# Kernel tuning notes

Hardware: AMD Instinct MI355X
Metric: run time of the kernel (lower is better)

## Reference

```python
import jax, jax.numpy as jnp
import numpy as np

N = 50000
E = 800000
IN_C = 128
OUT_C = 128
N_TYPES = 3
NEG_SLOPE = 0.2  # PyG GATConv default negative_slope


def setup_inputs() -> dict:
    key = jax.random.key(0)
    ks = jax.random.split(key, 10)
    x = jax.random.normal(ks[0], (N, IN_C), dtype=jnp.float32)
    edge_index = jax.random.randint(ks[1], (2, E), 0, N, dtype=jnp.int32)
    edge_type = jax.random.randint(ks[2], (E,), 0, N_TYPES, dtype=jnp.int32)
    node_type = jax.random.randint(ks[3], (N,), 0, 3, dtype=jnp.int32)
    s = 1.0 / np.sqrt(IN_C)
    emb_table = jax.random.normal(ks[4], (3, IN_C), dtype=jnp.float32)
    W = jax.random.normal(ks[5], (N_TYPES, IN_C, OUT_C), dtype=jnp.float32) * s
    att_src = jax.random.normal(ks[6], (N_TYPES, OUT_C), dtype=jnp.float32) * s
    att_dst = jax.random.normal(ks[7], (N_TYPES, OUT_C), dtype=jnp.float32) * s
    bias = jax.random.normal(ks[8], (N_TYPES, OUT_C), dtype=jnp.float32) * 0.01
    return {"x": x, "edge_index": edge_index, "edge_type": edge_type,
            "node_type": node_type, "emb_table": emb_table, "W": W,
            "att_src": att_src, "att_dst": att_dst, "bias": bias}


def reference(x, edge_index, edge_type, node_type, emb_table, W, att_src, att_dst, bias):
    # Eval mode: dropouts are identity. edge_index is non-empty -> GAT branch.
    n = x.shape[0]
    x = x + emb_table[node_type]  # node-type embedding add
    src, dst = edge_index[0], edge_index[1]
    out_sum = jnp.zeros((n, OUT_C), dtype=x.dtype)
    for t in range(N_TYPES):  # per-edge-type GATConv (heads=1, add_self_loops=True)
        xw = x @ W[t]                       # [N, out]
        a_s = xw @ att_src[t]               # [N] alpha_src per node
        a_d = xw @ att_dst[t]               # [N] alpha_dst per node
        mask = edge_type == t               # [E]
        e_raw = jax.nn.leaky_relu(a_s[src] + a_d[dst], NEG_SLOPE)  # [E]
        e_self = jax.nn.leaky_relu(a_s + a_d, NEG_SLOPE)           # [N] self-loop logit
        e_masked = jnp.where(mask, e_raw, -jnp.inf)
        m = jnp.maximum(jax.ops.segment_max(e_masked, dst, num_segments=n), e_self)
        m = jax.lax.stop_gradient(m)
        w_edge = jnp.where(mask, jnp.exp(e_raw - m[dst]), 0.0)     # [E]
        w_self = jnp.exp(e_self - m)                               # [N]
        denom = jax.ops.segment_sum(w_edge, dst, num_segments=n) + w_self
        num = jax.ops.segment_sum(w_edge[:, None] * xw[src], dst, num_segments=n) \
              + w_self[:, None] * xw
        out_sum = out_sum + num / denom[:, None] + bias[t]
        # (attention weights per type are w_edge/denom[dst]; only node output returned)
    return out_sum
```

## Files before the change

kernel.cpp:

```cpp
#include <hip/hip_runtime.h>
#include <math.h>

#define N_NODES 50000
#define N_EDGES 800000
#define C 128
#define NT 3
#define NEG 0.2f
#define CAP 64

#define GEMM_XB 782

typedef __attribute__((ext_vector_type(8))) short short8;
typedef __attribute__((ext_vector_type(4))) float f32x4;

__device__ __forceinline__ float leaky(float v) { return v > 0.f ? v : NEG * v; }

__device__ __forceinline__ unsigned short f2bf(float f) {
  unsigned int u = __float_as_uint(f);
  u = (u + 0x7FFFu + ((u >> 16) & 1u)) >> 16;
  return (unsigned short)u;
}
__device__ __forceinline__ float bf_lo(unsigned int w) { return __uint_as_float(w << 16); }
__device__ __forceinline__ float bf_hi(unsigned int w) { return __uint_as_float(w & 0xFFFF0000u); }

__global__ void k_wt(const float* __restrict__ W, unsigned short* __restrict__ Wt) {
  int idx = blockIdx.x * 256 + threadIdx.x;
  int t = idx >> 14, rem = idx & 16383;
  int n = rem >> 7, k = rem & 127;
  Wt[((size_t)t * C + n) * C + k] = f2bf(W[((size_t)t * C + k) * C + n]);
}

__global__ void k_main(const float* __restrict__ x, const int* __restrict__ node_type,
                       const float* __restrict__ emb, const unsigned short* __restrict__ Wt,
                       unsigned short* __restrict__ xwb,
                       const float* __restrict__ att_src, const float* __restrict__ att_dst,
                       float* __restrict__ a_s, float2* __restrict__ ad_es,
                       const int* __restrict__ ei, const int* __restrict__ etype,
                       int* __restrict__ cnt, int* __restrict__ buckets) {
  __shared__ unsigned short As[64][136];
  __shared__ unsigned short Bs[128][136];
  const int bid = blockIdx.x;
  const int r = bid & 3;
  const int tid = threadIdx.x;

  if (r == 3) {
    int e0 = ((bid >> 2) * 256 + tid) * 4;
    if (e0 + 4 <= N_EDGES) {
      int4 s4 = *(const int4*)(ei + e0);
      int4 d4 = *(const int4*)(ei + N_EDGES + e0);
      int4 t4 = *(const int4*)(etype + e0);
      int p0 = atomicAdd(&cnt[d4.x], 1);
      int p1 = atomicAdd(&cnt[d4.y], 1);
      int p2 = atomicAdd(&cnt[d4.z], 1);
      int p3 = atomicAdd(&cnt[d4.w], 1);
      if (p0 < CAP) buckets[(size_t)d4.x * CAP + p0] = t4.x * N_NODES + s4.x;
      if (p1 < CAP) buckets[(size_t)d4.y * CAP + p1] = t4.y * N_NODES + s4.y;
      if (p2 < CAP) buckets[(size_t)d4.z * CAP + p2] = t4.z * N_NODES + s4.z;
      if (p3 < CAP) buckets[(size_t)d4.w * CAP + p3] = t4.w * N_NODES + s4.w;
    }
    return;
  }

  const int wid = tid >> 6, lane = tid & 63;
  const int m = lane & 15, quad = lane >> 4;
  const int row0 = (bid >> 2) * 64;
  const int t = r;

#pragma unroll
  for (int it = 0; it < 8; ++it) {
    int c = tid + it * 256;
    int rr = c >> 5, q = c & 31;
    int row = row0 + rr;
    float4 xv = make_float4(0.f, 0.f, 0.f, 0.f);
    int nt = 0;
    if (row < N_NODES) {
      xv = *(const float4*)(x + (size_t)row * C + q * 4);
      nt = node_type[row];
    }
    float4 ev = ((const float4*)emb)[nt * 32 + q];
    ushort4 o;
    o.x = f2bf(xv.x + ev.x); o.y = f2bf(xv.y + ev.y);
    o.z = f2bf(xv.z + ev.z); o.w = f2bf(xv.w + ev.w);
    *(ushort4*)&As[rr][q * 4] = o;
  }
  const unsigned short* Wtt = Wt + (size_t)t * C * C;
#pragma unroll
  for (int it = 0; it < 8; ++it) {
    int c = tid + it * 256;
    int n = c >> 4, kc = c & 15;
    *(uint4*)&Bs[n][kc * 8] = *(const uint4*)(Wtt + (size_t)n * C + kc * 8);
  }
  __syncthreads();

  f32x4 acc[8] = {};
#pragma unroll
  for (int k0 = 0; k0 < 128; k0 += 32) {
    short8 a = *(const short8*)&As[wid * 16 + m][k0 + quad * 8];
#pragma unroll
    for (int j = 0; j < 8; ++j) {
      short8 b = *(const short8*)&Bs[j * 16 + m][k0 + quad * 8];
      acc[j] = __builtin_amdgcn_mfma_f32_16x16x32_bf16(a, b, acc[j], 0, 0, 0);
    }
  }

  float asv[8], adv[8];
#pragma unroll
  for (int j = 0; j < 8; ++j) {
    asv[j] = att_src[t * C + j * 16 + m];
    adv[j] = att_dst[t * C + j * 16 + m];
  }
  float ps[4] = {}, pd[4] = {};
#pragma unroll
  for (int j = 0; j < 8; ++j) {
#pragma unroll
    for (int reg = 0; reg < 4; ++reg) {
      int row = row0 + wid * 16 + quad * 4 + reg;
      float v = acc[j][reg];
      if (row < N_NODES) xwb[((size_t)t * N_NODES + row) * C + j * 16 + m] = f2bf(v);
      ps[reg] += v * asv[j];
      pd[reg] += v * adv[j];
    }
  }
#pragma unroll
  for (int off = 1; off < 16; off <<= 1) {
#pragma unroll
    for (int reg = 0; reg < 4; ++reg) {
      ps[reg] += __shfl_xor(ps[reg], off);
      pd[reg] += __shfl_xor(pd[reg], off);
    }
  }
  if (m == 0) {
#pragma unroll
    for (int reg = 0; reg < 4; ++reg) {
      int row = row0 + wid * 16 + quad * 4 + reg;
      if (row < N_NODES) {
        int idx = t * N_NODES + row;
        a_s[idx] = ps[reg];
        ad_es[idx] = make_float2(pd[reg], leaky(ps[reg] + pd[reg]));
      }
    }
  }
}

__global__ void k_gather(const int* __restrict__ cnt, const int* __restrict__ buckets,
                         const unsigned short* __restrict__ xwb,
                         const float* __restrict__ a_s, const float2* __restrict__ ad_es,
                         const float* __restrict__ bias, float* __restrict__ out) {
  int wid = threadIdx.x >> 6;
  int lane = threadIdx.x & 63;
  int i = blockIdx.x * 4 + wid;
  if (i >= N_NODES) return;
  int n = cnt[i];
  if (n > CAP) n = CAP;

  int idxl = 0;
  if (lane < n) idxl = buckets[(size_t)i * CAP + lane];
  int tl = idxl >= 2 * N_NODES ? 2 : (idxl >= N_NODES ? 1 : 0);
  float as = a_s[idxl];
  float2 am = ad_es[tl * N_NODES + i];
  float wl = (lane < n) ? __expf(leaky(as + am.x) - am.y) : 0.f;

  float s0 = tl == 0 ? wl : 0.f;
  float s1 = tl == 1 ? wl : 0.f;
  float s2 = tl == 2 ? wl : 0.f;
#pragma unroll
  for (int off = 1; off < 64; off <<= 1) {
    s0 += __shfl_xor(s0, off);
    s1 += __shfl_xor(s1, off);
    s2 += __shfl_xor(s2, off);
  }
  float inv3[NT] = {1.f / (s0 + 1.f), 1.f / (s1 + 1.f), 1.f / (s2 + 1.f)};
  float wc = wl * inv3[tl];

  float acc0 = 0.f, acc1 = 0.f;
#pragma unroll
  for (int t = 0; t < NT; ++t) {
    int idx = t * N_NODES + i;
    float coef = inv3[t];
    unsigned int w = ((const unsigned int*)(xwb + (size_t)idx * C))[lane];
    float2 b2 = ((const float2*)(bias + t * C))[lane];
    acc0 += coef * bf_lo(w) + b2.x;
    acc1 += coef * bf_hi(w) + b2.y;
  }

  const unsigned int* xwu = (const unsigned int*)xwb;
  int j = 0;
  for (; j + 16 <= n; j += 16) {
    float ac0 = 0.f, ac1 = 0.f;
#pragma unroll
    for (int k = 0; k < 16; ++k) {
      int idx = __shfl(idxl, j + k);
      float c = __shfl(wc, j + k);
      unsigned int v = xwu[(size_t)idx * (C / 2) + lane];
      ac0 += c * bf_lo(v);
      ac1 += c * bf_hi(v);
    }
    acc0 += ac0; acc1 += ac1;
  }
  for (; j + 8 <= n; j += 8) {
    float ac0 = 0.f, ac1 = 0.f;
#pragma unroll
    for (int k = 0; k < 8; ++k) {
      int idx = __shfl(idxl, j + k);
      float c = __shfl(wc, j + k);
      unsigned int v = xwu[(size_t)idx * (C / 2) + lane];
      ac0 += c * bf_lo(v);
      ac1 += c * bf_hi(v);
    }
    acc0 += ac0; acc1 += ac1;
  }
  for (; j < n; ++j) {
    int idx = __shfl(idxl, j);
    float c = __shfl(wc, j);
    unsigned int v = xwu[(size_t)idx * (C / 2) + lane];
    acc0 += c * bf_lo(v);
    acc1 += c * bf_hi(v);
  }
  ((float2*)(out + (size_t)i * C))[lane] = make_float2(acc0, acc1);
}

extern "C" void kernel_launch(void* const* d_in, const int* in_sizes, int n_in,
                              void* d_out, int out_size, void* d_ws, size_t ws_size,
                              hipStream_t stream) {
  const float* x       = (const float*)d_in[0];
  const int* edge_idx  = (const int*)d_in[1];
  const int* edge_type = (const int*)d_in[2];
  const int* node_type = (const int*)d_in[3];
  const float* emb     = (const float*)d_in[4];
  const float* W       = (const float*)d_in[5];
  const float* att_src = (const float*)d_in[6];
  const float* att_dst = (const float*)d_in[7];
  const float* bias    = (const float*)d_in[8];
  float* out = (float*)d_out;

  unsigned short* xwb = (unsigned short*)d_ws;
  unsigned short* Wt  = xwb + (size_t)NT * N_NODES * C;
  float*  a_s   = (float*)(Wt + (size_t)NT * C * C);
  float2* ad_es = (float2*)(a_s + (size_t)NT * N_NODES);
  int*    cnt   = (int*)(ad_es + (size_t)NT * N_NODES);
  int*    buckets = (int*)(cnt + N_NODES);

  hipMemsetAsync(cnt, 0, N_NODES * sizeof(int), stream);
  k_wt<<<192, 256, 0, stream>>>(W, Wt);

  k_main<<<4 * GEMM_XB, 256, 0, stream>>>(x, node_type, emb, Wt, xwb, att_src, att_dst,
                                          a_s, ad_es, edge_idx, edge_type, cnt, buckets);

  k_gather<<<(N_NODES + 3) / 4, 256, 0, stream>>>(cnt, buckets, xwb, a_s, ad_es, bias, out);
}
```

Before: 195.1 us.

## Reuse input tile across all edge types and fold count reset into prep

The main kernel now loads and converts each 64-row x tile once into shared memory. It then loops over the three edge types, reloading only the per-type weight tile between them. Before, three separate blocks each re-read and re-converted the same x rows. The hipMemsetAsync of the per-node counters is folded into the weight-transpose kernel, removing one launch. The trade-off is fewer, longer GEMM blocks with extra barriers, which may reduce parallelism and latency hiding.

```diff
diff --git a/kernel.cpp b/kernel.cpp
--- a/kernel.cpp
+++ b/kernel.cpp
@@ -23,11 +23,18 @@
 __device__ __forceinline__ float bf_lo(unsigned int w) { return __uint_as_float(w << 16); }
 __device__ __forceinline__ float bf_hi(unsigned int w) { return __uint_as_float(w & 0xFFFF0000u); }
 
-__global__ void k_wt(const float* __restrict__ W, unsigned short* __restrict__ Wt) {
-  int idx = blockIdx.x * 256 + threadIdx.x;
-  int t = idx >> 14, rem = idx & 16383;
-  int n = rem >> 7, k = rem & 127;
-  Wt[((size_t)t * C + n) * C + k] = f2bf(W[((size_t)t * C + k) * C + n]);
+__global__ void k_prep(const float* __restrict__ W, unsigned short* __restrict__ Wt,
+                       int* __restrict__ cnt) {
+  int bid = blockIdx.x;
+  if (bid < 192) {
+    int idx = bid * 256 + threadIdx.x;
+    int t = idx >> 14, rem = idx & 16383;
+    int n = rem >> 7, k = rem & 127;
+    Wt[((size_t)t * C + n) * C + k] = f2bf(W[((size_t)t * C + k) * C + n]);
+  } else {
+    int i4 = (bid - 192) * 256 + threadIdx.x;
+    if (i4 < N_NODES / 4) ((int4*)cnt)[i4] = make_int4(0, 0, 0, 0);
+  }
 }
 
 __global__ void k_main(const float* __restrict__ x, const int* __restrict__ node_type,
@@ -40,11 +47,10 @@
   __shared__ unsigned short As[64][136];
   __shared__ unsigned short Bs[128][136];
   const int bid = blockIdx.x;
-  const int r = bid & 3;
   const int tid = threadIdx.x;
 
-  if (r == 3) {
-    int e0 = ((bid >> 2) * 256 + tid) * 4;
+  if (bid & 1) {
+    int e0 = ((bid >> 1) * 256 + tid) * 4;
     if (e0 + 4 <= N_EDGES) {
       int4 s4 = *(const int4*)(ei + e0);
       int4 d4 = *(const int4*)(ei + N_EDGES + e0);
@@ -63,8 +69,7 @@
 
   const int wid = tid >> 6, lane = tid & 63;
   const int m = lane & 15, quad = lane >> 4;
-  const int row0 = (bid >> 2) * 64;
-  const int t = r;
+  const int row0 = (bid >> 1) * 64;
 
 #pragma unroll
   for (int it = 0; it < 8; ++it) {
@@ -83,61 +88,70 @@
     o.z = f2bf(xv.z + ev.z); o.w = f2bf(xv.w + ev.w);
     *(ushort4*)&As[rr][q * 4] = o;
   }
-  const unsigned short* Wtt = Wt + (size_t)t * C * C;
 #pragma unroll
   for (int it = 0; it < 8; ++it) {
     int c = tid + it * 256;
     int n = c >> 4, kc = c & 15;
-    *(uint4*)&Bs[n][kc * 8] = *(const uint4*)(Wtt + (size_t)n * C + kc * 8);
+    *(uint4*)&Bs[n][kc * 8] = *(const uint4*)(Wt + (size_t)n * C + kc * 8);
   }
   __syncthreads();
 
-  f32x4 acc[8] = {};
-#pragma unroll
-  for (int k0 = 0; k0 < 128; k0 += 32) {
-    short8 a = *(const short8*)&As[wid * 16 + m][k0 + quad * 8];
+  for (int t = 0; t < NT; ++t) {
+    f32x4 acc[8] = {};
+#pragma unroll
+    for (int k0 = 0; k0 < 128; k0 += 32) {
+      short8 a = *(const short8*)&As[wid * 16 + m][k0 + quad * 8];
+#pragma unroll
+      for (int j = 0; j < 8; ++j) {
+        short8 b = *(const short8*)&Bs[j * 16 + m][k0 + quad * 8];
+        acc[j] = __builtin_amdgcn_mfma_f32_16x16x32_bf16(a, b, acc[j], 0, 0, 0);
+      }
+    }
+
+    float ps[4] = {}, pd[4] = {};
 #pragma unroll
     for (int j = 0; j < 8; ++j) {
-      short8 b = *(const short8*)&Bs[j * 16 + m][k0 + quad * 8];
-      acc[j] = __builtin_amdgcn_mfma_f32_16x16x32_bf16(a, b, acc[j], 0, 0, 0);
-    }
-  }
-
-  float asv[8], adv[8];
-#pragma unroll
-  for (int j = 0; j < 8; ++j) {
-    asv[j] = att_src[t * C + j * 16 + m];
-    adv[j] = att_dst[t * C + j * 16 + m];
-  }
-  float ps[4] = {}, pd[4] = {};
-#pragma unroll
-  for (int j = 0; j < 8; ++j) {
-#pragma unroll
-    for (int reg = 0; reg < 4; ++reg) {
-      int row = row0 + wid * 16 + quad * 4 + reg;
-      float v = acc[j][reg];
-      if (row < N_NODES) xwb[((size_t)t * N_NODES + row) * C + j * 16 + m] = f2bf(v);
-      ps[reg] += v * asv[j];
-      pd[reg] += v * adv[j];
-    }
-  }
-#pragma unroll
-  for (int off = 1; off < 16; off <<= 1) {
-#pragma unroll
-    for (int reg = 0; reg < 4; ++reg) {
-      ps[reg] += __shfl_xor(ps[reg], off);
-      pd[reg] += __shfl_xor(pd[reg], off);
-    }
-  }
-  if (m == 0) {
-#pragma unroll
-    for (int reg = 0; reg < 4; ++reg) {
-      int row = row0 + wid * 16 + quad * 4 + reg;
-      if (row < N_NODES) {
-        int idx = t * N_NODES + row;
-        a_s[idx] = ps[reg];
-        ad_es[idx] = make_float2(pd[reg], leaky(ps[reg] + pd[reg]));
-      }
+      float as = att_src[t * C + j * 16 + m];
+      float ad = att_dst[t * C + j * 16 + m];
+#pragma unroll
+      for (int reg = 0; reg < 4; ++reg) {
+        int row = row0 + wid * 16 + quad * 4 + reg;
+        float v = acc[j][reg];
+        if (row < N_NODES) xwb[((size_t)t * N_NODES + row) * C + j * 16 + m] = f2bf(v);
+        ps[reg] += v * as;
+        pd[reg] += v * ad;
+      }
+    }
+#pragma unroll
+    for (int off = 1; off < 16; off <<= 1) {
+#pragma unroll
+      for (int reg = 0; reg < 4; ++reg) {
+        ps[reg] += __shfl_xor(ps[reg], off);
+        pd[reg] += __shfl_xor(pd[reg], off);
+      }
+    }
+    if (m == 0) {
+#pragma unroll
+      for (int reg = 0; reg < 4; ++reg) {
+        int row = row0 + wid * 16 + quad * 4 + reg;
+        if (row < N_NODES) {
+          int idx = t * N_NODES + row;
+          a_s[idx] = ps[reg];
+          ad_es[idx] = make_float2(pd[reg], leaky(ps[reg] + pd[reg]));
+        }
+      }
+    }
+
+    if (t + 1 < NT) {
+      __syncthreads();
+      const unsigned short* Wtt = Wt + (size_t)(t + 1) * C * C;
+#pragma unroll
+      for (int it = 0; it < 8; ++it) {
+        int c = tid + it * 256;
+        int n = c >> 4, kc = c & 15;
+        *(uint4*)&Bs[n][kc * 8] = *(const uint4*)(Wtt + (size_t)n * C + kc * 8);
+      }
+      __syncthreads();
     }
   }
 }
@@ -240,10 +254,9 @@
   int*    cnt   = (int*)(ad_es + (size_t)NT * N_NODES);
   int*    buckets = (int*)(cnt + N_NODES);
 
-  hipMemsetAsync(cnt, 0, N_NODES * sizeof(int), stream);
-  k_wt<<<192, 256, 0, stream>>>(W, Wt);
-
-  k_main<<<4 * GEMM_XB, 256, 0, stream>>>(x, node_type, emb, Wt, xwb, att_src, att_dst,
+  k_prep<<<192 + 49, 256, 0, stream>>>(W, Wt, cnt);
+
+  k_main<<<2 * GEMM_XB, 256, 0, stream>>>(x, node_type, emb, Wt, xwb, att_src, att_dst,
                                           a_s, ad_es, edge_idx, edge_type, cnt, buckets);
 
   k_gather<<<(N_NODES + 3) / 4, 256, 0, stream>>>(cnt, buckets, xwb, a_s, ad_es, bias, out);
```

After: 189.5 us. 2.9% less time.
